# Kernel tuning notes

Measured on AMD Instinct MI355X. Metric: run time of the kernel, lower is better.

The kernel has to match this reference:

```python
import jax, jax.numpy as jnp
import numpy as np

B, N, M = 8, 8192, 2048
C1, C2 = 128, 256
H = 256  # mlp hidden/out channels


def setup_inputs() -> dict:
    key = jax.random.key(0)
    ks = jax.random.split(key, 8)
    return {
        "unknown": jax.random.normal(ks[0], (B, N, 3), dtype=jnp.float32),
        "known": jax.random.normal(ks[1], (B, M, 3), dtype=jnp.float32),
        "unknow_feats": jax.random.normal(ks[2], (B, C1, N), dtype=jnp.float32),
        "known_feats": jax.random.normal(ks[3], (B, C2, M), dtype=jnp.float32),
        "W1": jax.random.normal(ks[4], (H, C1 + C2), dtype=jnp.float32) * 0.02,
        "b1": jnp.zeros((H,), dtype=jnp.float32),
        "W2": jax.random.normal(ks[5], (H, H), dtype=jnp.float32) * 0.02,
        "b2": jnp.zeros((H,), dtype=jnp.float32),
    }


def _three_nn(unknown, known):
    # squared pairwise distances (B, n, m)
    d2 = jnp.sum((unknown[:, :, None, :] - known[:, None, :, :]) ** 2, axis=-1)
    neg_d2_top, idx = jax.lax.top_k(-d2, 3)  # 3 smallest distances
    dist = jnp.sqrt(jnp.maximum(-neg_d2_top, 0.0))  # (B, n, 3)
    return dist, idx


def _three_interpolate(features, idx, weight):
    # features: (B, c, m); idx, weight: (B, n, 3) -> (B, c, n)
    Bc, c, m = features.shape
    n = idx.shape[1]
    idx_flat = jnp.broadcast_to(idx.reshape(Bc, 1, n * 3), (Bc, c, n * 3))
    gathered = jnp.take_along_axis(features, idx_flat, axis=2).reshape(Bc, c, n, 3)
    return jnp.sum(gathered * weight[:, None, :, :], axis=-1)


def reference(unknown, known, unknow_feats, known_feats, W1, b1, W2, b2):
    dist, idx = _three_nn(unknown, known)
    dist_recip = 1.0 / (dist + 1e-8)
    weight = dist_recip / jnp.sum(dist_recip, axis=2, keepdims=True)  # (B, n, 3)
    interpolated = _three_interpolate(known_feats, idx, weight)  # (B, C2, n)
    new_features = jnp.concatenate([interpolated, unknow_feats], axis=1)  # (B, C1+C2, n)
    # shared MLP: two conv1x1 (bias, no BN) + ReLU
    h = jax.nn.relu(jnp.einsum('oc,bcn->bon', W1, new_features) + b1[None, :, None])
    out = jax.nn.relu(jnp.einsum('oc,bcn->bon', W2, h) + b2[None, :, None])
    return out
```

## Files before the change

kernel.cpp:

```cpp
#include <hip/hip_runtime.h>

using bf16x8 = __attribute__((ext_vector_type(8))) short;
using f32x4  = __attribute__((ext_vector_type(4))) float;
using f32x2  = __attribute__((ext_vector_type(2))) float;

constexpr int Bb = 8, Nn = 8192, Mm = 2048, C1 = 128, C2 = 256, Hh = 256, K1 = 384;
constexpr int KT1 = K1 / 32;
constexpr int KT2 = Hh / 32;
constexpr int RT = Hh / 16;
constexpr int NQ = 4;
constexpr int MQ = Mm / NQ;

__device__ __forceinline__ short f2bf(float x) {
  union { float f; unsigned u; } v; v.f = x;
  unsigned r = v.u + 0x7fff + ((v.u >> 16) & 1);
  return (short)(r >> 16);
}

__device__ __forceinline__ unsigned pk2bf(float a, float b) {
#if defined(__has_builtin) && __has_builtin(__builtin_amdgcn_cvt_pk_bf16_f32)
  typedef __attribute__((ext_vector_type(2))) __bf16 bf2_t;
  bf2_t r = __builtin_amdgcn_cvt_pk_bf16_f32(a, b);
  union { bf2_t v; unsigned u; } cvt; cvt.v = r;
  return cvt.u;
#else
  return (unsigned)(unsigned short)f2bf(a) | ((unsigned)(unsigned short)f2bf(b) << 16);
#endif
}

__device__ __forceinline__ float bflo(unsigned d) { return __uint_as_float(d << 16); }
__device__ __forceinline__ float bfhi(unsigned d) { return __uint_as_float(d & 0xffff0000u); }

__device__ __forceinline__ f32x2 pk_add(f32x2 a, f32x2 b) {
  f32x2 d; asm("v_pk_add_f32 %0, %1, %2" : "=v"(d) : "v"(a), "v"(b)); return d;
}
__device__ __forceinline__ f32x2 pk_mul(f32x2 a, f32x2 b) {
  f32x2 d; asm("v_pk_mul_f32 %0, %1, %2" : "=v"(d) : "v"(a), "v"(b)); return d;
}
__device__ __forceinline__ f32x2 pk_fma(f32x2 a, f32x2 b, f32x2 c) {
  f32x2 d; asm("v_pk_fma_f32 %0, %1, %2, %3" : "=v"(d) : "v"(a), "v"(b), "v"(c)); return d;
}

__device__ __forceinline__ void merge3(float a0, float a1, float a2, int A0, int A1, int A2,
                                       float b0, float b1, float b2, int B0, int B1, int B2,
                                       float& m0, float& m1, float& m2,
                                       int& j0, int& j1, int& j2) {
  bool ta = a0 <= b0;
  m0 = ta ? a0 : b0; j0 = ta ? A0 : B0;
  float na0 = ta ? a1 : a0, na1 = ta ? a2 : a1;
  int   nA0 = ta ? A1 : A0, nA1 = ta ? A2 : A1;
  float nb0 = ta ? b0 : b1, nb1 = ta ? b1 : b2;
  int   nB0 = ta ? B0 : B1, nB1 = ta ? B1 : B2;
  ta = na0 <= nb0;
  m1 = ta ? na0 : nb0; j1 = ta ? nA0 : nB0;
  float ma0 = ta ? na1 : na0; int mA0 = ta ? nA1 : nA0;
  float mb0 = ta ? nb0 : nb1; int mB0 = ta ? nB0 : nB1;
  ta = ma0 <= mb0;
  m2 = ta ? ma0 : mb0; j2 = ta ? mA0 : mB0;
}

__global__ __launch_bounds__(256) void prep_all_k(const float* __restrict__ kf,
                                                  short* __restrict__ kfTb,
                                                  const float* __restrict__ W1,
                                                  const float* __restrict__ W2,
                                                  short* __restrict__ W1f,
                                                  short* __restrict__ W2f) {
  __shared__ float tile[32][33];
  int bid = blockIdx.x, tid = threadIdx.x;
  if (bid < 4096) {
    int cx = bid & 63, ry = (bid >> 6) & 7, z = bid >> 9;
    const float* src = kf + (size_t)z * C2 * Mm;
    short* dst = kfTb + (size_t)z * Mm * C2;
    int c0 = cx * 32, r0 = ry * 32;
    int tx = tid & 31, ty = tid >> 5;
#pragma unroll
    for (int rr = ty; rr < 32; rr += 8)
      tile[rr][tx] = src[(size_t)(r0 + rr) * Mm + c0 + tx];
    __syncthreads();
#pragma unroll
    for (int cc = ty; cc < 32; cc += 8)
      dst[(size_t)(c0 + cc) * C2 + r0 + tx] = f2bf(tile[tx][cc]);
    return;
  }
  int id = (bid - 4096) * 256 + tid;
  const int n1 = KT1 * RT * 64;
  const int n2 = KT2 * RT * 64;
  if (id < n1) {
    int lane = id & 63, t = id >> 6;
    int kt = t / RT, rt = t % RT;
    int m = rt * 16 + (lane & 15), k0 = kt * 32 + (lane >> 4) * 8;
    bf16x8 f;
#pragma unroll
    for (int j = 0; j < 8; ++j) f[j] = f2bf(W1[(size_t)m * K1 + k0 + j]);
    *(bf16x8*)(W1f + (size_t)id * 8) = f;
  } else if (id < n1 + n2) {
    int id2 = id - n1;
    int lane = id2 & 63, t = id2 >> 6;
    int kt = t / RT, rt = t % RT;
    int m = rt * 16 + (lane & 15), k0 = kt * 32 + (lane >> 4) * 8;
    bf16x8 f;
#pragma unroll
    for (int j = 0; j < 8; ++j) f[j] = f2bf(W2[(size_t)m * Hh + k0 + j]);
    *(bf16x8*)(W2f + (size_t)id2 * 8) = f;
  }
}

__global__ __launch_bounds__(256) void nn_quarter_k(const float* __restrict__ unknown,
                                                    const float* __restrict__ known,
                                                    float* __restrict__ pd,
                                                    int* __restrict__ pi) {
  __shared__ float kx[MQ], ky[MQ], kz[MQ];
  int bid = blockIdx.x;
  int b = bid >> 7, rem = bid & 127;
  int q = rem & 3, nblk = rem >> 2;
  int n = nblk * 256 + threadIdx.x;
  const float* kb = known + ((size_t)b * Mm + q * MQ) * 3;
  for (int p = threadIdx.x; p < MQ; p += 256) {
    kx[p] = kb[3 * p]; ky[p] = kb[3 * p + 1]; kz[p] = kb[3 * p + 2];
  }
  __syncthreads();

  size_t ui = ((size_t)b * Nn + n) * 3;
  float ux = unknown[ui], uy = unknown[ui + 1], uz = unknown[ui + 2];
  float d0 = 1e30f, d1 = 1e30f, d2 = 1e30f;
  int i0 = 0, i1 = 0, i2 = 0;
  int gbase = q * MQ;

  f32x2 nux = { -ux, -ux }, nuy = { -uy, -uy }, nuz = { -uz, -uz };

#define NN_INS(dd, qq)                                                  \
  {                                                                     \
    if (__any((dd) < d2)) {  \
      int jm = gbase + jb + (qq);                                       \
      bool c0 = (dd) < d0, c1 = (dd) < d1, c2 = (dd) < d2;              \
      d2 = c1 ? d1 : (c2 ? (dd) : d2); i2 = c1 ? i1 : (c2 ? jm : i2);   \
      d1 = c0 ? d0 : (c1 ? (dd) : d1); i1 = c0 ? i0 : (c1 ? jm : i1);   \
      d0 = c0 ? (dd) : d0;             i0 = c0 ? jm : i0;               \
    }                                                                   \
  }

  const f32x2* kx2 = (const f32x2*)kx;
  const f32x2* ky2 = (const f32x2*)ky;
  const f32x2* kz2 = (const f32x2*)kz;
  for (int jb = 0; jb < MQ; jb += 4) {
    int h = jb >> 1;
    f32x2 xa = kx2[h], xb = kx2[h + 1];
    f32x2 ya = ky2[h], yb = ky2[h + 1];
    f32x2 za = kz2[h], zb = kz2[h + 1];
    f32x2 dxa = pk_add(xa, nux), dya = pk_add(ya, nuy), dza = pk_add(za, nuz);
    f32x2 dda = pk_fma(dza, dza, pk_fma(dya, dya, pk_mul(dxa, dxa)));
    f32x2 dxb = pk_add(xb, nux), dyb = pk_add(yb, nuy), dzb = pk_add(zb, nuz);
    f32x2 ddb = pk_fma(dzb, dzb, pk_fma(dyb, dyb, pk_mul(dxb, dxb)));
    NN_INS(dda.x, 0)
    NN_INS(dda.y, 1)
    NN_INS(ddb.x, 2)
    NN_INS(ddb.y, 3)
  }
#undef NN_INS

  size_t o = (((size_t)b * Nn + n) * NQ + q) * 3;
  pd[o] = d0; pd[o + 1] = d1; pd[o + 2] = d2;
  pi[o] = i0; pi[o + 1] = i1; pi[o + 2] = i2;
}

__global__ __launch_bounds__(256) void fused_gemm_k(
    const float* __restrict__ uf, const short* __restrict__ kfTb,
    const short* __restrict__ W1f, const float* __restrict__ b1,
    const short* __restrict__ W2f, const float* __restrict__ b2,
    const float* __restrict__ pd, const int* __restrict__ pi,
    float* __restrict__ out) {
  __shared__ short Fs[KT2 * 4 * 64 * 8];
  short* Hs = Fs;
  int bid = blockIdx.x;
  int b = bid >> 7, bt = bid & 127;
  int tid = threadIdx.x, lane = tid & 63, wv = tid >> 6;
  int quad = lane >> 4, col = lane & 15;
  const int nq = bt * 64 + wv * 16 + col;

  float w0, w1, w2;
  int g0, g1, g2;
  {
    size_t pbase = (size_t)(b * Nn + nq) * (NQ * 3);
    float4 da = *(const float4*)&pd[pbase];
    float4 db = *(const float4*)&pd[pbase + 4];
    float4 dc = *(const float4*)&pd[pbase + 8];
    int4 ia = *(const int4*)&pi[pbase];
    int4 ib = *(const int4*)&pi[pbase + 4];
    int4 ic = *(const int4*)&pi[pbase + 8];
    float t0, t1, t2, u0, u1, u2, m0, m1, m2;
    int T0, T1, T2, U0, U1, U2;
    merge3(da.x, da.y, da.z, ia.x, ia.y, ia.z,
           da.w, db.x, db.y, ia.w, ib.x, ib.y, t0, t1, t2, T0, T1, T2);
    merge3(db.z, db.w, dc.x, ib.z, ib.w, ic.x,
           dc.y, dc.z, dc.w, ic.y, ic.z, ic.w, u0, u1, u2, U0, U1, U2);
    merge3(t0, t1, t2, T0, T1, T2, u0, u1, u2, U0, U1, U2,
           m0, m1, m2, g0, g1, g2);
    float s0 = sqrtf(m0), s1 = sqrtf(m1), s2 = sqrtf(m2);
    float r0 = 1.f / (s0 + 1e-8f), r1 = 1.f / (s1 + 1e-8f), r2 = 1.f / (s2 + 1e-8f);
    float rs = 1.f / (r0 + r1 + r2);
    w0 = r0 * rs; w1 = r1 * rs; w2 = r2 * rs;
  }
  const short* kfb = kfTb + (size_t)b * Mm * C2;

#define GATHER_KT(kt, plane)                                                  \
  {                                                                           \
    int c0 = (kt) * 32 + quad * 8;                                            \
    uint4 q0 = *(const uint4*)&kfb[(size_t)g0 * C2 + c0];                     \
    uint4 q1 = *(const uint4*)&kfb[(size_t)g1 * C2 + c0];                     \
    uint4 q2 = *(const uint4*)&kfb[(size_t)g2 * C2 + c0];                     \
    float e0 = w0 * bflo(q0.x) + w1 * bflo(q1.x) + w2 * bflo(q2.x);           \
    float e1 = w0 * bfhi(q0.x) + w1 * bfhi(q1.x) + w2 * bfhi(q2.x);           \
    float e2 = w0 * bflo(q0.y) + w1 * bflo(q1.y) + w2 * bflo(q2.y);           \
    float e3 = w0 * bfhi(q0.y) + w1 * bfhi(q1.y) + w2 * bfhi(q2.y);           \
    float e4 = w0 * bflo(q0.z) + w1 * bflo(q1.z) + w2 * bflo(q2.z);           \
    float e5 = w0 * bfhi(q0.z) + w1 * bfhi(q1.z) + w2 * bfhi(q2.z);           \
    float e6 = w0 * bflo(q0.w) + w1 * bflo(q1.w) + w2 * bflo(q2.w);           \
    float e7 = w0 * bfhi(q0.w) + w1 * bfhi(q1.w) + w2 * bfhi(q2.w);           \
    uint4 packed;                                                             \
    packed.x = pk2bf(e0, e1); packed.y = pk2bf(e2, e3);                       \
    packed.z = pk2bf(e4, e5); packed.w = pk2bf(e6, e7);                       \
    *(uint4*)&Fs[(((plane) * 4 + wv) * 64 + lane) * 8] = packed;              \
  }

#pragma unroll 3
  for (int kt = 0; kt < 6; ++kt) GATHER_KT(kt, kt)
  __syncthreads();

  f32x4 acc[4][4];
#pragma unroll
  for (int r = 0; r < 4; ++r)
#pragma unroll
    for (int c = 0; c < 4; ++c) acc[r][c] = (f32x4){0.f, 0.f, 0.f, 0.f};

  for (int kt = 0; kt < 6; ++kt) {
    bf16x8 Afr[4], Bfr[4];
#pragma unroll
    for (int r = 0; r < 4; ++r)
      Afr[r] = *(const bf16x8*)(W1f + ((size_t)(kt * RT + wv * 4 + r) * 64 + lane) * 8);
#pragma unroll
    for (int c = 0; c < 4; ++c)
      Bfr[c] = *(const bf16x8*)&Fs[((kt * 4 + c) * 64 + lane) * 8];
#pragma unroll
    for (int r = 0; r < 4; ++r)
#pragma unroll
      for (int c = 0; c < 4; ++c)
        acc[r][c] = __builtin_amdgcn_mfma_f32_16x16x32_bf16(Afr[r], Bfr[c], acc[r][c], 0, 0, 0);
  }
  __syncthreads();

  GATHER_KT(6, 0)
  GATHER_KT(7, 1)
#pragma unroll 2
  for (int kt = 8; kt < 12; ++kt) {
    int c1 = (kt - 8) * 32 + quad * 8;
    float e[8];
#pragma unroll
    for (int j = 0; j < 8; ++j)
      e[j] = uf[((size_t)b * C1 + c1 + j) * Nn + nq];
    uint4 packed;
    packed.x = pk2bf(e[0], e[1]); packed.y = pk2bf(e[2], e[3]);
    packed.z = pk2bf(e[4], e[5]); packed.w = pk2bf(e[6], e[7]);
    *(uint4*)&Fs[(((kt - 6) * 4 + wv) * 64 + lane) * 8] = packed;
  }
#undef GATHER_KT
  __syncthreads();

  for (int kt = 6; kt < KT1; ++kt) {
    bf16x8 Afr[4], Bfr[4];
#pragma unroll
    for (int r = 0; r < 4; ++r)
      Afr[r] = *(const bf16x8*)(W1f + ((size_t)(kt * RT + wv * 4 + r) * 64 + lane) * 8);
#pragma unroll
    for (int c = 0; c < 4; ++c)
      Bfr[c] = *(const bf16x8*)&Fs[(((kt - 6) * 4 + c) * 64 + lane) * 8];
#pragma unroll
    for (int r = 0; r < 4; ++r)
#pragma unroll
      for (int c = 0; c < 4; ++c)
        acc[r][c] = __builtin_amdgcn_mfma_f32_16x16x32_bf16(Afr[r], Bfr[c], acc[r][c], 0, 0, 0);
  }

#pragma unroll
  for (int r = 0; r < 4; ++r) {
    f32x4 bq = *(const f32x4*)&b1[wv * 64 + r * 16 + quad * 4];
#pragma unroll
    for (int c = 0; c < 4; ++c)
#pragma unroll
      for (int reg = 0; reg < 4; ++reg)
        acc[r][c][reg] = fmaxf(acc[r][c][reg] + bq[reg], 0.f);
  }
  __syncthreads();
  {
    int addr_lo = (((quad & 1) * 2) * 16 + col) * 4;
    bool hiSel = lane >= 32;
#pragma unroll
    for (int ktl = 0; ktl < 2; ++ktl)
#pragma unroll
      for (int c = 0; c < 4; ++c) {
        float e[8];
#pragma unroll
        for (int j = 0; j < 8; ++j) {
          int addr = addr_lo + (j >> 2) * 64;
          int lo = __builtin_amdgcn_ds_bpermute(addr, __float_as_int(acc[ktl * 2][c][j & 3]));
          int hi = __builtin_amdgcn_ds_bpermute(addr, __float_as_int(acc[ktl * 2 + 1][c][j & 3]));
          e[j] = __int_as_float(hiSel ? hi : lo);
        }
        uint4 packed;
        packed.x = pk2bf(e[0], e[1]); packed.y = pk2bf(e[2], e[3]);
        packed.z = pk2bf(e[4], e[5]); packed.w = pk2bf(e[6], e[7]);
        *(uint4*)&Hs[(((wv * 2 + ktl) * 4 + c) * 64 + lane) * 8] = packed;
      }
  }
  __syncthreads();

  f32x4 acc2[4][4];
#pragma unroll
  for (int r = 0; r < 4; ++r)
#pragma unroll
    for (int c = 0; c < 4; ++c) acc2[r][c] = (f32x4){0.f, 0.f, 0.f, 0.f};

  for (int kt = 0; kt < KT2; ++kt) {
    bf16x8 Afr[4], Bfr[4];
#pragma unroll
    for (int r = 0; r < 4; ++r)
      Afr[r] = *(const bf16x8*)(W2f + ((size_t)(kt * RT + wv * 4 + r) * 64 + lane) * 8);
#pragma unroll
    for (int c = 0; c < 4; ++c)
      Bfr[c] = *(const bf16x8*)&Hs[((kt * 4 + c) * 64 + lane) * 8];
#pragma unroll
    for (int r = 0; r < 4; ++r)
#pragma unroll
      for (int c = 0; c < 4; ++c)
        acc2[r][c] = __builtin_amdgcn_mfma_f32_16x16x32_bf16(Afr[r], Bfr[c], acc2[r][c], 0, 0, 0);
  }

#pragma unroll
  for (int r = 0; r < 4; ++r) {
    f32x4 bq = *(const f32x4*)&b2[wv * 64 + r * 16 + quad * 4];
#pragma unroll
    for (int c = 0; c < 4; ++c)
#pragma unroll
      for (int reg = 0; reg < 4; ++reg) {
        int rowg = wv * 64 + r * 16 + quad * 4 + reg;
        int n = bt * 64 + c * 16 + col;
        out[((size_t)b * Hh + rowg) * Nn + n] = fmaxf(acc2[r][c][reg] + bq[reg], 0.f);
      }
  }
}

extern "C" void kernel_launch(void* const* d_in, const int* in_sizes, int n_in,
                              void* d_out, int out_size, void* d_ws, size_t ws_size,
                              hipStream_t stream) {
  const float* unknown = (const float*)d_in[0];
  const float* known   = (const float*)d_in[1];
  const float* uf      = (const float*)d_in[2];
  const float* kf      = (const float*)d_in[3];
  const float* W1      = (const float*)d_in[4];
  const float* b1      = (const float*)d_in[5];
  const float* W2      = (const float*)d_in[6];
  const float* b2      = (const float*)d_in[7];
  float* out = (float*)d_out;

  char* p = (char*)d_ws;
  short* kfTb = (short*)p; p += (size_t)Bb * Mm * C2 * 2;
  short* W1f = (short*)p;  p += (size_t)KT1 * RT * 64 * 8 * 2;
  short* W2f = (short*)p;  p += (size_t)KT2 * RT * 64 * 8 * 2;
  float* pd  = (float*)p;  p += (size_t)Bb * Nn * NQ * 3 * 4;
  int* pi    = (int*)p;    p += (size_t)Bb * Nn * NQ * 3 * 4;

  const int prep_blocks = 4096 + (KT1 * RT * 64 + KT2 * RT * 64 + 255) / 256;
  prep_all_k<<<dim3(prep_blocks), dim3(256), 0, stream>>>(kf, kfTb, W1, W2, W1f, W2f);
  nn_quarter_k<<<dim3(Bb * 32 * NQ), dim3(256), 0, stream>>>(unknown, known, pd, pi);
  fused_gemm_k<<<dim3(Bb * (Nn / 64)), dim3(256), 0, stream>>>(
      uf, kfTb, W1f, b1, W2f, b2, pd, pi, out);
}
```

Before: 216.8 us.

## Halve point tile per block to 32 and split gather across wave pairs

The fused GEMM kernel now covers 32 points per block instead of 64, which doubles the grid to 2048 blocks. Each pair of waves shares a 16-point sub-tile and splits the gather/K-planes between them. This cuts per-block LDS and accumulator registers and should raise occupancy and parallelism. In exchange, every block re-reads the full W1/W2 fragments for half as many points, doubling weight traffic per output, and the MFMA issue per A-fragment load drops.

```diff
diff --git a/kernel.cpp b/kernel.cpp
--- a/kernel.cpp
+++ b/kernel.cpp
@@ -8,6 +8,7 @@
 constexpr int KT1 = K1 / 32;
 constexpr int KT2 = Hh / 32;
 constexpr int RT = Hh / 16;
+constexpr int NTL = 2;
 constexpr int NQ = 4;
 constexpr int MQ = Mm / NQ;
 
@@ -169,13 +170,15 @@
     const short* __restrict__ W2f, const float* __restrict__ b2,
     const float* __restrict__ pd, const int* __restrict__ pi,
     float* __restrict__ out) {
-  __shared__ short Fs[KT2 * 4 * 64 * 8];
+  __shared__ short Fs[KT2 * NTL * 64 * 8];
   short* Hs = Fs;
   int bid = blockIdx.x;
-  int b = bid >> 7, bt = bid & 127;
+  int b = bid >> 8, bt = bid & 255;
   int tid = threadIdx.x, lane = tid & 63, wv = tid >> 6;
   int quad = lane >> 4, col = lane & 15;
-  const int nq = bt * 64 + wv * 16 + col;
+  const int ntl = wv & 1;
+  const int kph = wv >> 1;
+  const int nq = bt * 32 + ntl * 16 + col;
 
   float w0, w1, w2;
   int g0, g1, g2;
@@ -219,39 +222,42 @@
     uint4 packed;                                                             \
     packed.x = pk2bf(e0, e1); packed.y = pk2bf(e2, e3);                       \
     packed.z = pk2bf(e4, e5); packed.w = pk2bf(e6, e7);                       \
-    *(uint4*)&Fs[(((plane) * 4 + wv) * 64 + lane) * 8] = packed;              \
-  }
-
-#pragma unroll 3
-  for (int kt = 0; kt < 6; ++kt) GATHER_KT(kt, kt)
-  __syncthreads();
-
-  f32x4 acc[4][4];
+    *(uint4*)&Fs[(((plane) * NTL + ntl) * 64 + lane) * 8] = packed;           \
+  }
+
+#pragma unroll
+  for (int it = 0; it < 3; ++it) {
+    int ktg = it * 2 + kph;
+    GATHER_KT(ktg, ktg)
+  }
+  __syncthreads();
+
+  f32x4 acc[4][NTL];
 #pragma unroll
   for (int r = 0; r < 4; ++r)
 #pragma unroll
-    for (int c = 0; c < 4; ++c) acc[r][c] = (f32x4){0.f, 0.f, 0.f, 0.f};
+    for (int c = 0; c < NTL; ++c) acc[r][c] = (f32x4){0.f, 0.f, 0.f, 0.f};
 
   for (int kt = 0; kt < 6; ++kt) {
-    bf16x8 Afr[4], Bfr[4];
+    bf16x8 Afr[4], Bfr[NTL];
 #pragma unroll
     for (int r = 0; r < 4; ++r)
       Afr[r] = *(const bf16x8*)(W1f + ((size_t)(kt * RT + wv * 4 + r) * 64 + lane) * 8);
 #pragma unroll
-    for (int c = 0; c < 4; ++c)
-      Bfr[c] = *(const bf16x8*)&Fs[((kt * 4 + c) * 64 + lane) * 8];
-#pragma unroll
-    for (int r = 0; r < 4; ++r)
-#pragma unroll
-      for (int c = 0; c < 4; ++c)
+    for (int c = 0; c < NTL; ++c)
+      Bfr[c] = *(const bf16x8*)&Fs[((kt * NTL + c) * 64 + lane) * 8];
+#pragma unroll
+    for (int r = 0; r < 4; ++r)
+#pragma unroll
+      for (int c = 0; c < NTL; ++c)
         acc[r][c] = __builtin_amdgcn_mfma_f32_16x16x32_bf16(Afr[r], Bfr[c], acc[r][c], 0, 0, 0);
   }
   __syncthreads();
 
-  GATHER_KT(6, 0)
-  GATHER_KT(7, 1)
-#pragma unroll 2
-  for (int kt = 8; kt < 12; ++kt) {
+  GATHER_KT(6 + kph, kph)
+#pragma unroll
+  for (int it = 0; it < 2; ++it) {
+    int kt = 8 + it * 2 + kph;
     int c1 = (kt - 8) * 32 + quad * 8;
     float e[8];
 #pragma unroll
@@ -260,23 +266,23 @@
     uint4 packed;
     packed.x = pk2bf(e[0], e[1]); packed.y = pk2bf(e[2], e[3]);
     packed.z = pk2bf(e[4], e[5]); packed.w = pk2bf(e[6], e[7]);
-    *(uint4*)&Fs[(((kt - 6) * 4 + wv) * 64 + lane) * 8] = packed;
+    *(uint4*)&Fs[(((kt - 6) * NTL + ntl) * 64 + lane) * 8] = packed;
   }
 #undef GATHER_KT
   __syncthreads();
 
   for (int kt = 6; kt < KT1; ++kt) {
-    bf16x8 Afr[4], Bfr[4];
+    bf16x8 Afr[4], Bfr[NTL];
 #pragma unroll
     for (int r = 0; r < 4; ++r)
       Afr[r] = *(const bf16x8*)(W1f + ((size_t)(kt * RT + wv * 4 + r) * 64 + lane) * 8);
 #pragma unroll
-    for (int c = 0; c < 4; ++c)
-      Bfr[c] = *(const bf16x8*)&Fs[(((kt - 6) * 4 + c) * 64 + lane) * 8];
-#pragma unroll
-    for (int r = 0; r < 4; ++r)
-#pragma unroll
-      for (int c = 0; c < 4; ++c)
+    for (int c = 0; c < NTL; ++c)
+      Bfr[c] = *(const bf16x8*)&Fs[(((kt - 6) * NTL + c) * 64 + lane) * 8];
+#pragma unroll
+    for (int r = 0; r < 4; ++r)
+#pragma unroll
+      for (int c = 0; c < NTL; ++c)
         acc[r][c] = __builtin_amdgcn_mfma_f32_16x16x32_bf16(Afr[r], Bfr[c], acc[r][c], 0, 0, 0);
   }
 
@@ -284,7 +290,7 @@
   for (int r = 0; r < 4; ++r) {
     f32x4 bq = *(const f32x4*)&b1[wv * 64 + r * 16 + quad * 4];
 #pragma unroll
-    for (int c = 0; c < 4; ++c)
+    for (int c = 0; c < NTL; ++c)
 #pragma unroll
       for (int reg = 0; reg < 4; ++reg)
         acc[r][c][reg] = fmaxf(acc[r][c][reg] + bq[reg], 0.f);
@@ -296,7 +302,7 @@
 #pragma unroll
     for (int ktl = 0; ktl < 2; ++ktl)
 #pragma unroll
-      for (int c = 0; c < 4; ++c) {
+      for (int c = 0; c < NTL; ++c) {
         float e[8];
 #pragma unroll
         for (int j = 0; j < 8; ++j) {
@@ -308,29 +314,29 @@
         uint4 packed;
         packed.x = pk2bf(e[0], e[1]); packed.y = pk2bf(e[2], e[3]);
         packed.z = pk2bf(e[4], e[5]); packed.w = pk2bf(e[6], e[7]);
-        *(uint4*)&Hs[(((wv * 2 + ktl) * 4 + c) * 64 + lane) * 8] = packed;
+        *(uint4*)&Hs[(((wv * 2 + ktl) * NTL + c) * 64 + lane) * 8] = packed;
       }
   }
   __syncthreads();
 
-  f32x4 acc2[4][4];
+  f32x4 acc2[4][NTL];
 #pragma unroll
   for (int r = 0; r < 4; ++r)
 #pragma unroll
-    for (int c = 0; c < 4; ++c) acc2[r][c] = (f32x4){0.f, 0.f, 0.f, 0.f};
+    for (int c = 0; c < NTL; ++c) acc2[r][c] = (f32x4){0.f, 0.f, 0.f, 0.f};
 
   for (int kt = 0; kt < KT2; ++kt) {
-    bf16x8 Afr[4], Bfr[4];
+    bf16x8 Afr[4], Bfr[NTL];
 #pragma unroll
     for (int r = 0; r < 4; ++r)
       Afr[r] = *(const bf16x8*)(W2f + ((size_t)(kt * RT + wv * 4 + r) * 64 + lane) * 8);
 #pragma unroll
-    for (int c = 0; c < 4; ++c)
-      Bfr[c] = *(const bf16x8*)&Hs[((kt * 4 + c) * 64 + lane) * 8];
-#pragma unroll
-    for (int r = 0; r < 4; ++r)
-#pragma unroll
-      for (int c = 0; c < 4; ++c)
+    for (int c = 0; c < NTL; ++c)
+      Bfr[c] = *(const bf16x8*)&Hs[((kt * NTL + c) * 64 + lane) * 8];
+#pragma unroll
+    for (int r = 0; r < 4; ++r)
+#pragma unroll
+      for (int c = 0; c < NTL; ++c)
         acc2[r][c] = __builtin_amdgcn_mfma_f32_16x16x32_bf16(Afr[r], Bfr[c], acc2[r][c], 0, 0, 0);
   }
 
@@ -338,11 +344,11 @@
   for (int r = 0; r < 4; ++r) {
     f32x4 bq = *(const f32x4*)&b2[wv * 64 + r * 16 + quad * 4];
 #pragma unroll
-    for (int c = 0; c < 4; ++c)
+    for (int c = 0; c < NTL; ++c)
 #pragma unroll
       for (int reg = 0; reg < 4; ++reg) {
         int rowg = wv * 64 + r * 16 + quad * 4 + reg;
-        int n = bt * 64 + c * 16 + col;
+        int n = bt * 32 + c * 16 + col;
         out[((size_t)b * Hh + rowg) * Nn + n] = fmaxf(acc2[r][c][reg] + bq[reg], 0.f);
       }
   }
@@ -371,6 +377,6 @@
   const int prep_blocks = 4096 + (KT1 * RT * 64 + KT2 * RT * 64 + 255) / 256;
   prep_all_k<<<dim3(prep_blocks), dim3(256), 0, stream>>>(kf, kfTb, W1, W2, W1f, W2f);
   nn_quarter_k<<<dim3(Bb * 32 * NQ), dim3(256), 0, stream>>>(unknown, known, pd, pi);
-  fused_gemm_k<<<dim3(Bb * (Nn / 64)), dim3(256), 0, stream>>>(
+  fused_gemm_k<<<dim3(Bb * (Nn / 32)), dim3(256), 0, stream>>>(
       uf, kfTb, W1f, b1, W2f, b2, pd, pi, out);
 }
```

New measurement: 249.6 us. 1.15x slower.
